# Kernel tuning notes

Measured on AMD Instinct MI355X. Metric: run time of the kernel, lower is better.

Reference implementation:

```python
import jax, jax.numpy as jnp
import numpy as np

N = 10000      # num_nodes (also input feature width per GCNConv(num_nodes, 200))
E = 320000     # num edges (avg degree 32)
H1 = 200
C = 8
N_TEST = 2000


def _gcn_norm(edge_index, edge_weight, num_nodes):
    """PyG GCNConv symmetric normalization with self-loops (fill value 1)."""
    loop = jnp.arange(num_nodes)
    row = jnp.concatenate([edge_index[0], loop])          # source nodes
    col = jnp.concatenate([edge_index[1], loop])          # target nodes
    w = jnp.concatenate([edge_weight, jnp.ones((num_nodes,), edge_weight.dtype)])
    deg = jax.ops.segment_sum(w, col, num_segments=num_nodes)
    dis = jnp.where(deg > 0, jax.lax.rsqrt(deg), 0.0)     # deg^{-1/2}, 0 for isolated
    norm = dis[row] * w * dis[col]
    return row, col, norm


def _gcn_conv(x, row, col, norm, W, b, num_nodes):
    h = x @ W                                             # linear transform first (PyG order)
    msg = h[row] * norm[:, None]                          # gather + scale
    out = jax.ops.segment_sum(msg, col, num_segments=num_nodes)  # scatter-add aggregate
    return out + b


def setup_inputs() -> dict:
    key = jax.random.key(0)
    ks = jax.random.split(key, 8)
    x = jax.random.normal(ks[0], (N, N), jnp.float32)
    edge_index = jax.random.randint(ks[1], (2, E), 0, N, dtype=jnp.int64) if jax.config.read('jax_enable_x64') else jax.random.randint(ks[1], (2, E), 0, N)
    edge_weight = jax.random.uniform(ks[2], (E,), jnp.float32)
    mask_idx = jax.random.randint(ks[3], (N_TEST,), 0, N)
    y = jax.random.randint(ks[4], (N,), 0, C)
    W1 = jax.random.normal(ks[5], (N, H1), jnp.float32) / np.sqrt(N).astype(np.float32)
    b1 = jnp.zeros((H1,), jnp.float32)
    W2 = jax.random.normal(ks[6], (H1, C), jnp.float32) / np.sqrt(H1).astype(np.float32)
    b2 = jnp.zeros((C,), jnp.float32)
    return {"x": x, "edge_index": edge_index, "edge_weight": edge_weight,
            "mask_idx": mask_idx, "y": y, "W1": W1, "b1": b1, "W2": W2, "b2": b2}


def reference(x, edge_index, edge_weight, mask_idx, y, W1, b1, W2, b2):
    row, col, norm = _gcn_norm(edge_index, edge_weight, N)
    h = _gcn_conv(x, row, col, norm, W1, b1, N)
    h = jax.nn.relu(h)
    # dropout: module run in eval mode -> identity
    h = _gcn_conv(h, row, col, norm, W2, b2, N)
    predictions = h[mask_idx]   # masked gather (mode='test')
    targets = y[mask_idx]
    return predictions, targets
```

## Files before the change

### kernel.cpp

```cpp
#include <hip/hip_runtime.h>
#include <hip/hip_bf16.h>

#define NN     10000
#define NE     320000
#define H1DIM  200
#define H1BST  208
#define NCLS   8
#define NTST   2000
#define KDIM   10000
#define KPAD   10048
#define KSPL   6
#define KSTEPS 26
#define NGEMMB 474

typedef __bf16 bf16x8 __attribute__((ext_vector_type(8)));
typedef float  f32x4  __attribute__((ext_vector_type(4)));

__device__ __forceinline__ void load_lds16(const void* g, void* l) {
  __builtin_amdgcn_global_load_lds(
      (__attribute__((address_space(1))) void*)(void*)g,
      (__attribute__((address_space(3))) void*)l, 16, 0, 0);
}


__global__ void k_prep0(float* deg, int* cnt, int* cur, int* flags,
                        const unsigned* ei, const unsigned* mk, const unsigned* yy,
                        const float* __restrict__ W1, __bf16* __restrict__ Wt) {
  __shared__ float tile[64][65];
  __shared__ int s_f[4];
  int b = blockIdx.x, t = threadIdx.x;
  if (b < 40) {
    int i = b * 256 + t;
    if (i < NN) { deg[i] = 1.0f; cnt[i] = 0; cur[i] = 0; }
    return;
  }
  if (b < 43) {
    unsigned a = 0;
    if (b == 40)      { for (int i = t; i < 2048; i += 256) a |= ei[2 * i + 1]; }
    else if (b == 41) { for (int i = t; i < 2048; i += 256) a |= yy[2 * i + 1]; }
    else              { for (int i = t; i < 900;  i += 256) a |= mk[2 * i + 1]; }
    int wid = t >> 6;
    int any = __any(a != 0) ? 1 : 0;
    if ((t & 63) == 0) s_f[wid] = any;
    __syncthreads();
    if (t == 0) {
      int f = s_f[0] | s_f[1] | s_f[2] | s_f[3];
      int idx = (b == 40) ? 0 : (b == 41) ? 2 : 1;
      flags[idx] = f;
    }
    return;
  }
  int bt = b - 43;
  int k0 = (bt % 157) * 64, n0 = (bt / 157) * 64;
  int tn = t & 63, tk = t >> 6;
  for (int r = 0; r < 64; r += 4) {
    int k = k0 + tk + r, n = n0 + tn;
    tile[tk + r][tn] = (k < KDIM && n < H1DIM) ? W1[k * H1DIM + n] : 0.f;
  }
  __syncthreads();
  for (int r = 0; r < 64; r += 4) {
    int n = n0 + tk + r, k = k0 + tn;
    if (k < KPAD && n < 256)
      Wt[(size_t)n * KPAD + k] = (__bf16)tile[tn][tk + r];
  }
}


__global__ void k_gemm_cvt(const float* __restrict__ x, const __bf16* __restrict__ Wt,
                           float* __restrict__ hpart,
                           const void* ei, const void* mk, const void* yy,
                           const float* __restrict__ ew, const int* __restrict__ flags,
                           int* idx32, int* mask32, int* y32, float* deg, int* cnt) {
  int t = threadIdx.x;
  if (blockIdx.x >= NGEMMB) {
    int i = (blockIdx.x - NGEMMB) * 512 + t;
    if (i < NE) {
      int v = (flags[0] == 0) ? (int)((const long long*)ei)[i] : ((const int*)ei)[i];
      idx32[i] = min(max(v, 0), NN - 1);
    } else if (i < 2 * NE) {
      int v = (flags[0] == 0) ? (int)((const long long*)ei)[i] : ((const int*)ei)[i];
      v = min(max(v, 0), NN - 1);
      idx32[i] = v;
      atomicAdd(&deg[v], ew[i - NE]);
      atomicAdd(&cnt[v], 1);
    } else if (i < 2 * NE + NTST) {
      int j = i - 2 * NE;
      int v = (flags[1] == 0) ? (int)((const long long*)mk)[j] : ((const int*)mk)[j];
      mask32[j] = min(max(v, 0), NN - 1);
    } else if (i < 2 * NE + NTST + NN) {
      int j = i - 2 * NE - NTST;
      int v = (flags[2] == 0) ? (int)((const long long*)yy)[j] : ((const int*)yy)[j];
      y32[j] = min(max(v, 0), NN - 1);
    }
    return;
  }

  __shared__ __align__(16) __bf16 As[128 * 64];
  __shared__ __align__(16) __bf16 Bs[256 * 64];
  int wv = t >> 6, lane = t & 63;
  int wm = wv >> 2, wn = wv & 3;
  int m0 = (blockIdx.x % 79) * 128;
  int split = blockIdx.x / 79;
  int kbeg = split * (KSTEPS * 64);
  int nsteps = KSTEPS + ((split == KSPL - 1) ? 1 : 0);

  f32x4 acc[4][4];
  #pragma unroll
  for (int i = 0; i < 4; ++i)
    #pragma unroll
    for (int j = 0; j < 4; ++j)
      #pragma unroll
      for (int r = 0; r < 4; ++r) acc[i][j][r] = 0.f;

  int am = t >> 2;
  int ac = t & 3;
  long arow = m0 + am; if (arow >= NN) arow = NN - 1;
  const float* aptr = x + (size_t)arow * KDIM + ac * 16;
  int ag0 = (2 * ac + 0) ^ (am & 7);
  int ag1 = (2 * ac + 1) ^ (am & 7);
  __bf16* awr0 = As + am * 64 + ag0 * 8;
  __bf16* awr1 = As + am * 64 + ag1 * 8;

  const __bf16* bsrc[4];
  __bf16* bdst[4];
  #pragma unroll
  for (int pass = 0; pass < 4; ++pass) {
    int s = pass * 512 + t;
    int brow = s >> 3, bg = s & 7;
    bsrc[pass] = Wt + (size_t)brow * KPAD + ((bg ^ (brow & 7)) * 8);
    bdst[pass] = Bs + (size_t)(pass * 512 + wv * 64) * 8;
  }

  int lrow = lane & 15;
  int lhi = lane >> 4;
  int lx7 = lane & 7;

  float4 v0, v1, v2, v3;
  {
    bool pr = (kbeg + ac * 16 + 16 <= KDIM);
    if (pr) {
      const float4* p = (const float4*)(aptr + kbeg);
      v0 = p[0]; v1 = p[1]; v2 = p[2]; v3 = p[3];
    }
  }

  for (int ks = 0; ks < nsteps; ++ks) {
    int k0 = kbeg + ks * 64;
    #pragma unroll
    for (int pass = 0; pass < 4; ++pass)
      load_lds16(bsrc[pass] + k0, bdst[pass]);
    {
      bool pr = (k0 + ac * 16 + 16 <= KDIM);
      bf16x8 bva, bvb;
      if (pr) {
        bva[0] = (__bf16)v0.x; bva[1] = (__bf16)v0.y;
        bva[2] = (__bf16)v0.z; bva[3] = (__bf16)v0.w;
        bva[4] = (__bf16)v1.x; bva[5] = (__bf16)v1.y;
        bva[6] = (__bf16)v1.z; bva[7] = (__bf16)v1.w;
        bvb[0] = (__bf16)v2.x; bvb[1] = (__bf16)v2.y;
        bvb[2] = (__bf16)v2.z; bvb[3] = (__bf16)v2.w;
        bvb[4] = (__bf16)v3.x; bvb[5] = (__bf16)v3.y;
        bvb[6] = (__bf16)v3.z; bvb[7] = (__bf16)v3.w;
      } else {
        #pragma unroll
        for (int q = 0; q < 8; ++q) { bva[q] = (__bf16)0.f; bvb[q] = (__bf16)0.f; }
      }
      *(bf16x8*)awr0 = bva;
      *(bf16x8*)awr1 = bvb;
    }
    __syncthreads();

    if (ks + 1 < nsteps) {
      int k1 = k0 + 64;
      bool pr = (k1 + ac * 16 + 16 <= KDIM);
      if (pr) {
        const float4* p = (const float4*)(aptr + k1);
        v0 = p[0]; v1 = p[1]; v2 = p[2]; v3 = p[3];
      }
    }

    #pragma unroll
    for (int kk = 0; kk < 2; ++kk) {
      int gs8 = ((kk * 4 + lhi) ^ lx7) * 8;
      bf16x8 af[4], bf[4];
      #pragma unroll
      for (int i = 0; i < 4; ++i)
        af[i] = *(const bf16x8*)&As[(wm * 64 + i * 16 + lrow) * 64 + gs8];
      #pragma unroll
      for (int j = 0; j < 4; ++j)
        bf[j] = *(const bf16x8*)&Bs[(wn * 64 + j * 16 + lrow) * 64 + gs8];
      #pragma unroll
      for (int i = 0; i < 4; ++i)
        #pragma unroll
        for (int j = 0; j < 4; ++j)
          acc[i][j] = __builtin_amdgcn_mfma_f32_16x16x32_bf16(af[i], bf[j], acc[i][j], 0, 0, 0);
    }
    __syncthreads();
  }

  float* outp = hpart + (size_t)split * NN * H1BST;
  int colb = wn * 64 + (lane & 15);
  int rbase = m0 + wm * 64 + ((lane >> 4) * 4);
  #pragma unroll
  for (int i = 0; i < 4; ++i)
    #pragma unroll
    for (int j = 0; j < 4; ++j) {
      int cg = colb + j * 16;
      if (cg < H1BST) {
        #pragma unroll
        for (int r = 0; r < 4; ++r) {
          int rg = rbase + i * 16 + r;
          if (rg < NN) outp[(size_t)rg * H1BST + cg] = acc[i][j][r];
        }
      }
    }
}


__global__ void k_scan_red(const int* __restrict__ cnt, const float* __restrict__ deg,
                           float* dis, int* rowptr,
                           const float* __restrict__ hpart, __bf16* __restrict__ h1b) {
  int t = threadIdx.x;
  if (blockIdx.x > 0) {
    int i = (blockIdx.x - 1) * 1024 + t;
    if (i < NN * 26) {
      int c = i / 26, ch = i - c * 26;
      size_t base = (size_t)c * H1BST + ch * 8;
      f32x4 s0, s1;
      #pragma unroll
      for (int q = 0; q < 4; ++q) { s0[q] = 0.f; s1[q] = 0.f; }
      #pragma unroll
      for (int sp = 0; sp < KSPL; ++sp) {
        const float* p = hpart + (size_t)sp * NN * H1BST + base;
        s0 += *(const f32x4*)p;
        s1 += *(const f32x4*)(p + 4);
      }
      bf16x8 o;
      o[0] = (__bf16)s0[0]; o[1] = (__bf16)s0[1]; o[2] = (__bf16)s0[2]; o[3] = (__bf16)s0[3];
      o[4] = (__bf16)s1[0]; o[5] = (__bf16)s1[1]; o[6] = (__bf16)s1[2]; o[7] = (__bf16)s1[3];
      *(bf16x8*)&h1b[(size_t)c * H1BST + ch * 8] = o;
    }
    return;
  }
  __shared__ int wsum[16];
  __shared__ int carry;
  int lane = t & 63, wid = t >> 6;
  if (t == 0) carry = 0;
  __syncthreads();
  for (int base = 0; base < NN; base += 1024) {
    int idx = base + t;
    if (idx < NN) { float d = deg[idx]; dis[idx] = (d > 0.f) ? rsqrtf(d) : 0.f; }
    int v = (idx < NN) ? cnt[idx] : 0;
    int x = v;
    #pragma unroll
    for (int off = 1; off < 64; off <<= 1) {
      int y = __shfl_up(x, off);
      if (lane >= off) x += y;
    }
    if (lane == 63) wsum[wid] = x;
    __syncthreads();
    int c0 = carry;
    if (t < 16) {
      int s = wsum[t];
      #pragma unroll
      for (int off = 1; off < 16; off <<= 1) {
        int y = __shfl_up(s, off);
        if (t >= off) s += y;
      }
      wsum[t] = s;
    }
    __syncthreads();
    int woff = (wid == 0) ? 0 : wsum[wid - 1];
    if (idx < NN) rowptr[idx] = c0 + woff + x - v;
    int tot = wsum[15];
    __syncthreads();
    if (t == 0) carry = c0 + tot;
    __syncthreads();
  }
  if (t == 0) rowptr[NN] = carry;
}

__global__ void k_norm_scatter(const int* __restrict__ rows, const int* __restrict__ cols,
                               const float* __restrict__ w, const float* __restrict__ dis,
                               const int* __restrict__ rowptr, int* cur,
                               float* normv, int* eids) {
  int e = blockIdx.x * 512 + threadIdx.x;
  if (e < NE) {
    int r = rows[e], c = cols[e];
    normv[e] = dis[r] * w[e] * dis[c];
    int pos = rowptr[c] + atomicAdd(&cur[c], 1);
    eids[pos] = e;
  }
}


__global__ void k_agg1lin2(const __bf16* __restrict__ h1b, const float* __restrict__ dis,
                           const float* __restrict__ normv, const int* __restrict__ rows,
                           const int* __restrict__ rowptr, const int* __restrict__ eids,
                           const float* __restrict__ b1, const float* __restrict__ W2,
                           float* __restrict__ h2) {
  __shared__ int   s_r[512];
  __shared__ float s_n[512];
  __shared__ float s_p[4][8];
  int c = blockIdx.x;
  int t = threadIdx.x;
  int lane = t & 63, wid = t >> 6;
  int p0 = rowptr[c], len = rowptr[c + 1] - p0;
  float acc = 0.f;
  for (int base = 0; base < len; base += 512) {
    int chunk = min(512, len - base);
    for (int j = t; j < chunk; j += 256) {
      int e = eids[p0 + base + j];
      s_r[j] = rows[e];
      s_n[j] = normv[e];
    }
    __syncthreads();
    if (t < H1DIM) {
      int j = 0;
      for (; j + 4 <= chunk; j += 4) {
        float v0 = s_n[j + 0] * (float)h1b[(size_t)s_r[j + 0] * H1BST + t];
        float v1 = s_n[j + 1] * (float)h1b[(size_t)s_r[j + 1] * H1BST + t];
        float v2 = s_n[j + 2] * (float)h1b[(size_t)s_r[j + 2] * H1BST + t];
        float v3 = s_n[j + 3] * (float)h1b[(size_t)s_r[j + 3] * H1BST + t];
        acc += v0 + v1 + v2 + v3;
      }
      for (; j < chunk; ++j) acc += s_n[j] * (float)h1b[(size_t)s_r[j] * H1BST + t];
    }
    __syncthreads();
  }
  float a = 0.f;
  if (t < H1DIM) {
    float d = dis[c];
    a = acc + d * d * (float)h1b[(size_t)c * H1BST + t] + b1[t];
    a = fmaxf(a, 0.f);
  }
  float p[8];
  if (t < H1DIM) {
    float4 w2a = *(const float4*)&W2[t * 8];
    float4 w2b = *(const float4*)&W2[t * 8 + 4];
    p[0] = a * w2a.x; p[1] = a * w2a.y; p[2] = a * w2a.z; p[3] = a * w2a.w;
    p[4] = a * w2b.x; p[5] = a * w2b.y; p[6] = a * w2b.z; p[7] = a * w2b.w;
  } else {
    #pragma unroll
    for (int o = 0; o < 8; ++o) p[o] = 0.f;
  }
  #pragma unroll
  for (int s = 32; s >= 1; s >>= 1) {
    #pragma unroll
    for (int o = 0; o < 8; ++o) p[o] += __shfl_down(p[o], s);
  }
  if (lane == 0) {
    #pragma unroll
    for (int o = 0; o < 8; ++o) s_p[wid][o] = p[o];
  }
  __syncthreads();
  if (t < 8)
    h2[(size_t)c * 8 + t] = s_p[0][t] + s_p[1][t] + s_p[2][t] + s_p[3][t];
}


__global__ void k_agg2out(const float* __restrict__ h2, const float* __restrict__ dis,
                          const float* __restrict__ normv, const int* __restrict__ rows,
                          const int* __restrict__ rowptr, const int* __restrict__ eids,
                          const float* __restrict__ b2, const int* __restrict__ mask,
                          const int* __restrict__ yv, float* __restrict__ out) {
  int i = blockIdx.x * 256 + threadIdx.x;
  if (i < NTST * NCLS) {
    int r = i >> 3, o = i & 7;
    int c = mask[r];
    float d = dis[c];
    float acc = d * d * h2[c * NCLS + o];
    int p0 = rowptr[c], p1 = rowptr[c + 1];
    for (int j = p0; j < p1; ++j) {
      int e = eids[j];
      acc += normv[e] * h2[rows[e] * NCLS + o];
    }
    out[i] = acc + b2[o];
  } else if (i < NTST * NCLS + NTST) {
    int r = i - NTST * NCLS;
    out[i] = (float)yv[mask[r]];
  }
}


extern "C" void kernel_launch(void* const* d_in, const int* in_sizes, int n_in,
                              void* d_out, int out_size, void* d_ws, size_t ws_size,
                              hipStream_t stream) {
  const float* x    = (const float*)d_in[0];
  const void*  ei   = d_in[1];
  const float* ew   = (const float*)d_in[2];
  const void*  mask = d_in[3];
  const void*  y    = d_in[4];
  const float* W1   = (const float*)d_in[5];
  const float* b1   = (const float*)d_in[6];
  const float* W2   = (const float*)d_in[7];
  const float* b2   = (const float*)d_in[8];
  float* out = (float*)d_out;

  char* ws = (char*)d_ws;
  float* deg    = (float*)(ws + 0);
  float* dis    = (float*)(ws + (64 << 10));
  float* normv  = (float*)(ws + (128 << 10));
  int*   idx32  = (int*)(ws + (2 << 20));
  float* h2     = (float*)(ws + (5 << 20));
  int*   mask32 = (int*)(ws + (6 << 20));
  int*   y32    = (int*)(ws + (6 << 20) + (64 << 10));
  int*   flags  = (int*)(ws + (6 << 20) + (128 << 10));
  int*   cnt    = (int*)(ws + (6 << 20) + (256 << 10));
  int*   cur    = (int*)(ws + (6 << 20) + (384 << 10));
  int*   rowptr = (int*)(ws + (6 << 20) + (512 << 10));
  int*   eids   = (int*)(ws + (7 << 20));
  __bf16* Wt    = (__bf16*)(ws + ((size_t)9 << 20));
  __bf16* h1b   = (__bf16*)(ws + ((size_t)16 << 20));
  float* hpart  = (float*)(ws + ((size_t)24 << 20));

  int* rows32 = idx32;
  int* cols32 = idx32 + NE;

  k_prep0<<<dim3(671), dim3(256), 0, stream>>>(deg, cnt, cur, flags,
                                               (const unsigned*)ei, (const unsigned*)mask,
                                               (const unsigned*)y, W1, Wt);

  k_gemm_cvt<<<dim3(NGEMMB + 1274), dim3(512), 0, stream>>>(
      x, Wt, hpart, ei, mask, y, ew, flags, idx32, mask32, y32, deg, cnt);

  k_scan_red<<<dim3(255), dim3(1024), 0, stream>>>(cnt, deg, dis, rowptr, hpart, h1b);

  k_norm_scatter<<<dim3(625), dim3(512), 0, stream>>>(rows32, cols32, ew, dis, rowptr, cur,
                                                      normv, eids);

  k_agg1lin2<<<dim3(10000), dim3(256), 0, stream>>>(h1b, dis, normv, rows32, rowptr, eids,
                                                    b1, W2, h2);
  k_agg2out<<<dim3(71), dim3(256), 0, stream>>>(h2, dis, normv, rows32, rowptr, eids, b2,
                                                mask32, y32, out);
}
```

Before: 259.8 us.

## Fuse post-GEMM stages into one cooperative kernel and store split-K partials as bf16

Four kernels (degree scan with split-K reduction, norm/CSR scatter, layer-1 aggregation with the W2 projection, layer-2 output gather) are merged into one persistent cooperative kernel of 256 blocks × 1024 threads, with grid.sync between phases. This removes separate launches and the gaps between them. The GEMM's split-K partial outputs are also written as bf16 instead of fp32, halving the traffic for writing and re-reading the partial buffer. In exchange, the aggregation phase now runs on far fewer, larger blocks and drops the LDS staging of edge indices, which may lower gather parallelism. Rounding partial sums to bf16 before reducing them also adds precision error.

```diff
diff --git a/kernel.cpp b/kernel.cpp
--- a/kernel.cpp
+++ b/kernel.cpp
@@ -1,5 +1,6 @@
 #include <hip/hip_runtime.h>
 #include <hip/hip_bf16.h>
+#include <hip/hip_cooperative_groups.h>
 
 #define NN     10000
 #define NE     320000
@@ -15,6 +16,8 @@
 
 typedef __bf16 bf16x8 __attribute__((ext_vector_type(8)));
 typedef float  f32x4  __attribute__((ext_vector_type(4)));
+
+namespace cg = cooperative_groups;
 
 __device__ __forceinline__ void load_lds16(const void* g, void* l) {
   __builtin_amdgcn_global_load_lds(
@@ -67,7 +70,7 @@
 
 
 __global__ void k_gemm_cvt(const float* __restrict__ x, const __bf16* __restrict__ Wt,
-                           float* __restrict__ hpart,
+                           __bf16* __restrict__ hpart,
                            const void* ei, const void* mk, const void* yy,
                            const float* __restrict__ ew, const int* __restrict__ flags,
                            int* idx32, int* mask32, int* y32, float* deg, int* cnt) {
@@ -198,7 +201,7 @@
     __syncthreads();
   }
 
-  float* outp = hpart + (size_t)split * NN * H1BST;
+  __bf16* outp = hpart + (size_t)split * NN * H1BST;
   int colb = wn * 64 + (lane & 15);
   int rbase = m0 + wm * 64 + ((lane >> 4) * 4);
   #pragma unroll
@@ -210,175 +213,165 @@
         #pragma unroll
         for (int r = 0; r < 4; ++r) {
           int rg = rbase + i * 16 + r;
-          if (rg < NN) outp[(size_t)rg * H1BST + cg] = acc[i][j][r];
+          if (rg < NN) outp[(size_t)rg * H1BST + cg] = (__bf16)acc[i][j][r];
         }
       }
     }
 }
 
 
-__global__ void k_scan_red(const int* __restrict__ cnt, const float* __restrict__ deg,
-                           float* dis, int* rowptr,
-                           const float* __restrict__ hpart, __bf16* __restrict__ h1b) {
-  int t = threadIdx.x;
-  if (blockIdx.x > 0) {
-    int i = (blockIdx.x - 1) * 1024 + t;
+struct CoopArgs {
+  const int* cnt; const float* deg; float* dis; int* rowptr;
+  const __bf16* hpart; __bf16* h1b;
+  const int* rows; const int* cols; const float* ew; int* cur;
+  float* normv; int* eids;
+  const float* b1; const float* W2; float* h2;
+  const float* b2; const int* mask; const int* yv; float* out;
+};
+
+__launch_bounds__(1024)
+__global__ void k_coop(CoopArgs a) {
+  cg::grid_group grid = cg::this_grid();
+  int b = blockIdx.x, t = threadIdx.x;
+
+  if (b == 0) {
+    __shared__ int wsum[16];
+    __shared__ int carry;
+    int lane = t & 63, wid = t >> 6;
+    if (t == 0) carry = 0;
+    __syncthreads();
+    for (int base = 0; base < NN; base += 1024) {
+      int idx = base + t;
+      if (idx < NN) { float d = a.deg[idx]; a.dis[idx] = (d > 0.f) ? rsqrtf(d) : 0.f; }
+      int v = (idx < NN) ? a.cnt[idx] : 0;
+      int x = v;
+      #pragma unroll
+      for (int off = 1; off < 64; off <<= 1) {
+        int y = __shfl_up(x, off);
+        if (lane >= off) x += y;
+      }
+      if (lane == 63) wsum[wid] = x;
+      __syncthreads();
+      int c0 = carry;
+      if (t < 16) {
+        int s = wsum[t];
+        #pragma unroll
+        for (int off = 1; off < 16; off <<= 1) {
+          int y = __shfl_up(s, off);
+          if (t >= off) s += y;
+        }
+        wsum[t] = s;
+      }
+      __syncthreads();
+      int woff = (wid == 0) ? 0 : wsum[wid - 1];
+      if (idx < NN) a.rowptr[idx] = c0 + woff + x - v;
+      int tot = wsum[15];
+      __syncthreads();
+      if (t == 0) carry = c0 + tot;
+      __syncthreads();
+    }
+    if (t == 0) a.rowptr[NN] = carry;
+  } else {
+    int i = (b - 1) * 1024 + t;
     if (i < NN * 26) {
       int c = i / 26, ch = i - c * 26;
       size_t base = (size_t)c * H1BST + ch * 8;
-      f32x4 s0, s1;
-      #pragma unroll
-      for (int q = 0; q < 4; ++q) { s0[q] = 0.f; s1[q] = 0.f; }
+      float s[8];
+      #pragma unroll
+      for (int q = 0; q < 8; ++q) s[q] = 0.f;
       #pragma unroll
       for (int sp = 0; sp < KSPL; ++sp) {
-        const float* p = hpart + (size_t)sp * NN * H1BST + base;
-        s0 += *(const f32x4*)p;
-        s1 += *(const f32x4*)(p + 4);
+        bf16x8 v = *(const bf16x8*)(a.hpart + (size_t)sp * NN * H1BST + base);
+        #pragma unroll
+        for (int q = 0; q < 8; ++q) s[q] += (float)v[q];
       }
       bf16x8 o;
-      o[0] = (__bf16)s0[0]; o[1] = (__bf16)s0[1]; o[2] = (__bf16)s0[2]; o[3] = (__bf16)s0[3];
-      o[4] = (__bf16)s1[0]; o[5] = (__bf16)s1[1]; o[6] = (__bf16)s1[2]; o[7] = (__bf16)s1[3];
-      *(bf16x8*)&h1b[(size_t)c * H1BST + ch * 8] = o;
-    }
-    return;
-  }
-  __shared__ int wsum[16];
-  __shared__ int carry;
-  int lane = t & 63, wid = t >> 6;
-  if (t == 0) carry = 0;
-  __syncthreads();
-  for (int base = 0; base < NN; base += 1024) {
-    int idx = base + t;
-    if (idx < NN) { float d = deg[idx]; dis[idx] = (d > 0.f) ? rsqrtf(d) : 0.f; }
-    int v = (idx < NN) ? cnt[idx] : 0;
-    int x = v;
-    #pragma unroll
-    for (int off = 1; off < 64; off <<= 1) {
-      int y = __shfl_up(x, off);
-      if (lane >= off) x += y;
-    }
-    if (lane == 63) wsum[wid] = x;
-    __syncthreads();
-    int c0 = carry;
-    if (t < 16) {
-      int s = wsum[t];
-      #pragma unroll
-      for (int off = 1; off < 16; off <<= 1) {
-        int y = __shfl_up(s, off);
-        if (t >= off) s += y;
-      }
-      wsum[t] = s;
-    }
-    __syncthreads();
-    int woff = (wid == 0) ? 0 : wsum[wid - 1];
-    if (idx < NN) rowptr[idx] = c0 + woff + x - v;
-    int tot = wsum[15];
-    __syncthreads();
-    if (t == 0) carry = c0 + tot;
-    __syncthreads();
-  }
-  if (t == 0) rowptr[NN] = carry;
-}
-
-__global__ void k_norm_scatter(const int* __restrict__ rows, const int* __restrict__ cols,
-                               const float* __restrict__ w, const float* __restrict__ dis,
-                               const int* __restrict__ rowptr, int* cur,
-                               float* normv, int* eids) {
-  int e = blockIdx.x * 512 + threadIdx.x;
-  if (e < NE) {
-    int r = rows[e], c = cols[e];
-    normv[e] = dis[r] * w[e] * dis[c];
-    int pos = rowptr[c] + atomicAdd(&cur[c], 1);
-    eids[pos] = e;
-  }
-}
-
-
-__global__ void k_agg1lin2(const __bf16* __restrict__ h1b, const float* __restrict__ dis,
-                           const float* __restrict__ normv, const int* __restrict__ rows,
-                           const int* __restrict__ rowptr, const int* __restrict__ eids,
-                           const float* __restrict__ b1, const float* __restrict__ W2,
-                           float* __restrict__ h2) {
-  __shared__ int   s_r[512];
-  __shared__ float s_n[512];
-  __shared__ float s_p[4][8];
-  int c = blockIdx.x;
-  int t = threadIdx.x;
-  int lane = t & 63, wid = t >> 6;
-  int p0 = rowptr[c], len = rowptr[c + 1] - p0;
-  float acc = 0.f;
-  for (int base = 0; base < len; base += 512) {
-    int chunk = min(512, len - base);
-    for (int j = t; j < chunk; j += 256) {
-      int e = eids[p0 + base + j];
-      s_r[j] = rows[e];
-      s_n[j] = normv[e];
-    }
-    __syncthreads();
-    if (t < H1DIM) {
-      int j = 0;
-      for (; j + 4 <= chunk; j += 4) {
-        float v0 = s_n[j + 0] * (float)h1b[(size_t)s_r[j + 0] * H1BST + t];
-        float v1 = s_n[j + 1] * (float)h1b[(size_t)s_r[j + 1] * H1BST + t];
-        float v2 = s_n[j + 2] * (float)h1b[(size_t)s_r[j + 2] * H1BST + t];
-        float v3 = s_n[j + 3] * (float)h1b[(size_t)s_r[j + 3] * H1BST + t];
-        acc += v0 + v1 + v2 + v3;
-      }
-      for (; j < chunk; ++j) acc += s_n[j] * (float)h1b[(size_t)s_r[j] * H1BST + t];
-    }
-    __syncthreads();
-  }
-  float a = 0.f;
-  if (t < H1DIM) {
-    float d = dis[c];
-    a = acc + d * d * (float)h1b[(size_t)c * H1BST + t] + b1[t];
-    a = fmaxf(a, 0.f);
-  }
-  float p[8];
-  if (t < H1DIM) {
-    float4 w2a = *(const float4*)&W2[t * 8];
-    float4 w2b = *(const float4*)&W2[t * 8 + 4];
-    p[0] = a * w2a.x; p[1] = a * w2a.y; p[2] = a * w2a.z; p[3] = a * w2a.w;
-    p[4] = a * w2b.x; p[5] = a * w2b.y; p[6] = a * w2b.z; p[7] = a * w2b.w;
-  } else {
-    #pragma unroll
-    for (int o = 0; o < 8; ++o) p[o] = 0.f;
-  }
-  #pragma unroll
-  for (int s = 32; s >= 1; s >>= 1) {
-    #pragma unroll
-    for (int o = 0; o < 8; ++o) p[o] += __shfl_down(p[o], s);
-  }
-  if (lane == 0) {
-    #pragma unroll
-    for (int o = 0; o < 8; ++o) s_p[wid][o] = p[o];
-  }
-  __syncthreads();
-  if (t < 8)
-    h2[(size_t)c * 8 + t] = s_p[0][t] + s_p[1][t] + s_p[2][t] + s_p[3][t];
-}
-
-
-__global__ void k_agg2out(const float* __restrict__ h2, const float* __restrict__ dis,
-                          const float* __restrict__ normv, const int* __restrict__ rows,
-                          const int* __restrict__ rowptr, const int* __restrict__ eids,
-                          const float* __restrict__ b2, const int* __restrict__ mask,
-                          const int* __restrict__ yv, float* __restrict__ out) {
-  int i = blockIdx.x * 256 + threadIdx.x;
-  if (i < NTST * NCLS) {
-    int r = i >> 3, o = i & 7;
-    int c = mask[r];
-    float d = dis[c];
-    float acc = d * d * h2[c * NCLS + o];
-    int p0 = rowptr[c], p1 = rowptr[c + 1];
-    for (int j = p0; j < p1; ++j) {
-      int e = eids[j];
-      acc += normv[e] * h2[rows[e] * NCLS + o];
-    }
-    out[i] = acc + b2[o];
-  } else if (i < NTST * NCLS + NTST) {
-    int r = i - NTST * NCLS;
-    out[i] = (float)yv[mask[r]];
+      #pragma unroll
+      for (int q = 0; q < 8; ++q) o[q] = (__bf16)s[q];
+      *(bf16x8*)&a.h1b[base] = o;
+    }
+  }
+  grid.sync();
+
+  for (int e = b * 1024 + t; e < NE; e += 256 * 1024) {
+    int r = a.rows[e], c = a.cols[e];
+    a.normv[e] = a.dis[r] * a.ew[e] * a.dis[c];
+    int pos = a.rowptr[c] + atomicAdd(&a.cur[c], 1);
+    a.eids[pos] = e;
+  }
+  grid.sync();
+
+  {
+    __shared__ float s_p[16][8];
+    int slot = t >> 8;
+    int ts = t & 255;
+    int gslot = b * 4 + slot;
+    for (int k = 0; k < 10; ++k) {
+      int c = gslot + k * 1024;
+      bool live = (c < NN);
+      float acc = 0.f;
+      if (live) {
+        int p0 = a.rowptr[c], p1 = a.rowptr[c + 1];
+        if (ts < H1DIM) {
+          for (int j = p0; j < p1; ++j) {
+            int e = a.eids[j];
+            acc += a.normv[e] * (float)a.h1b[(size_t)a.rows[e] * H1BST + ts];
+          }
+        }
+      }
+      float aval = 0.f;
+      if (live && ts < H1DIM) {
+        float d = a.dis[c];
+        aval = acc + d * d * (float)a.h1b[(size_t)c * H1BST + ts] + a.b1[ts];
+        aval = fmaxf(aval, 0.f);
+      }
+      float p[8];
+      if (live && ts < H1DIM) {
+        float4 w2a = *(const float4*)&a.W2[ts * 8];
+        float4 w2b = *(const float4*)&a.W2[ts * 8 + 4];
+        p[0] = aval * w2a.x; p[1] = aval * w2a.y; p[2] = aval * w2a.z; p[3] = aval * w2a.w;
+        p[4] = aval * w2b.x; p[5] = aval * w2b.y; p[6] = aval * w2b.z; p[7] = aval * w2b.w;
+      } else {
+        #pragma unroll
+        for (int o = 0; o < 8; ++o) p[o] = 0.f;
+      }
+      #pragma unroll
+      for (int s = 32; s >= 1; s >>= 1) {
+        #pragma unroll
+        for (int o = 0; o < 8; ++o) p[o] += __shfl_down(p[o], s);
+      }
+      int wid = t >> 6;
+      if ((t & 63) == 0) {
+        #pragma unroll
+        for (int o = 0; o < 8; ++o) s_p[wid][o] = p[o];
+      }
+      __syncthreads();
+      if (live && ts < 8) {
+        int wb = slot * 4;
+        a.h2[(size_t)c * 8 + ts] = s_p[wb][ts] + s_p[wb + 1][ts] + s_p[wb + 2][ts] + s_p[wb + 3][ts];
+      }
+      __syncthreads();
+    }
+  }
+  grid.sync();
+
+  {
+    int i = b * 1024 + t;
+    if (i < NTST * NCLS) {
+      int r = i >> 3, o = i & 7;
+      int c = a.mask[r];
+      float d = a.dis[c];
+      float acc = d * d * a.h2[c * NCLS + o];
+      int p0 = a.rowptr[c], p1 = a.rowptr[c + 1];
+      for (int j = p0; j < p1; ++j) {
+        int e = a.eids[j];
+        acc += a.normv[e] * a.h2[a.rows[e] * NCLS + o];
+      }
+      a.out[i] = acc + a.b2[o];
+    } else if (i < NTST * NCLS + NTST) {
+      int r = i - NTST * NCLS;
+      a.out[i] = (float)a.yv[a.mask[r]];
+    }
   }
 }
 
@@ -412,7 +405,7 @@
   int*   eids   = (int*)(ws + (7 << 20));
   __bf16* Wt    = (__bf16*)(ws + ((size_t)9 << 20));
   __bf16* h1b   = (__bf16*)(ws + ((size_t)16 << 20));
-  float* hpart  = (float*)(ws + ((size_t)24 << 20));
+  __bf16* hpart = (__bf16*)(ws + ((size_t)24 << 20));
 
   int* rows32 = idx32;
   int* cols32 = idx32 + NE;
@@ -424,13 +417,13 @@
   k_gemm_cvt<<<dim3(NGEMMB + 1274), dim3(512), 0, stream>>>(
       x, Wt, hpart, ei, mask, y, ew, flags, idx32, mask32, y32, deg, cnt);
 
-  k_scan_red<<<dim3(255), dim3(1024), 0, stream>>>(cnt, deg, dis, rowptr, hpart, h1b);
-
-  k_norm_scatter<<<dim3(625), dim3(512), 0, stream>>>(rows32, cols32, ew, dis, rowptr, cur,
-                                                      normv, eids);
-
-  k_agg1lin2<<<dim3(10000), dim3(256), 0, stream>>>(h1b, dis, normv, rows32, rowptr, eids,
-                                                    b1, W2, h2);
-  k_agg2out<<<dim3(71), dim3(256), 0, stream>>>(h2, dis, normv, rows32, rowptr, eids, b2,
-                                                mask32, y32, out);
+  CoopArgs ca;
+  ca.cnt = cnt; ca.deg = deg; ca.dis = dis; ca.rowptr = rowptr;
+  ca.hpart = hpart; ca.h1b = h1b;
+  ca.rows = rows32; ca.cols = cols32; ca.ew = ew; ca.cur = cur;
+  ca.normv = normv; ca.eids = eids;
+  ca.b1 = b1; ca.W2 = W2; ca.h2 = h2;
+  ca.b2 = b2; ca.mask = mask32; ca.yv = y32; ca.out = out;
+  void* params[] = { &ca };
+  hipLaunchCooperativeKernel((const void*)k_coop, dim3(256), dim3(1024), params, 0, stream);
 }
```

After: 561.6 us. 2.16x slower.
